# Kernel optimization log

Measured on AMD Instinct MI355X. Metric: run time of the kernel, lower is better.

Reference implementation:

```python
import jax, jax.numpy as jnp
import numpy as np

B, S, HID = 1, 2048, 2048
H, KV, D = 16, 4, 128  # head_dim = HID // H; GQA group size g = H // KV
THETA = 10000.0


def setup_inputs() -> dict:
    key = jax.random.key(0)
    ks = jax.random.split(key, 5)
    s = 0.02  # initializer_range
    return {
        "hidden_states": jax.random.normal(ks[0], (B, S, HID), jnp.float32),
        "wq": jax.random.normal(ks[1], (HID, H * D), jnp.float32) * s,
        "wk": jax.random.normal(ks[2], (HID, KV * D), jnp.float32) * s,
        "wv": jax.random.normal(ks[3], (HID, KV * D), jnp.float32) * s,
        "wo": jax.random.normal(ks[4], (H * D, HID), jnp.float32) * s,
        "attention_mask": jnp.ones((B, S), jnp.int32),
        "position_ids": jnp.broadcast_to(jnp.arange(S, dtype=jnp.int32), (B, S)),
    }


def _rope(x, position_ids):
    # x: [b, s, h, d]; rotate consecutive (even, odd) pairs by angle t * theta^{-2j/d}
    half = D // 2
    inv_freq = 1.0 / (THETA ** (jnp.arange(0, D, 2, dtype=jnp.float32) / D))  # [half]
    ang = position_ids[..., None].astype(jnp.float32) * inv_freq  # [b, s, half]
    cos = jnp.cos(ang)[:, :, None, :]  # [b, s, 1, half]
    sin = jnp.sin(ang)[:, :, None, :]
    xr = x.astype(jnp.float32).reshape(*x.shape[:-1], half, 2)
    x0, x1 = xr[..., 0], xr[..., 1]
    out = jnp.stack((x0 * cos - x1 * sin, x0 * sin + x1 * cos), axis=-1)
    return out.reshape(x.shape)


def reference(hidden_states, wq, wk, wv, wo, attention_mask, position_ids):
    b, s, _ = hidden_states.shape
    g = H // KV
    xq = (hidden_states @ wq).reshape(b, s, H, D)
    xk = (hidden_states @ wk).reshape(b, s, KV, D)
    xv = (hidden_states @ wv).reshape(b, s, KV, D)
    # GQA: each kv head repeated g consecutive times -> H heads (matches einops '(h g)')
    xk = jnp.repeat(xk, g, axis=2)
    xv = jnp.repeat(xv, g, axis=2)
    xq = _rope(xq, position_ids)
    xk = _rope(xk, position_ids)
    # causal + padding mask -> additive bias (0 or -inf), softmax in fp32
    causal = jnp.tril(jnp.ones((s, s), dtype=bool))[None, None]  # [1,1,q,k]
    mask = causal & (attention_mask[:, None, None, :] > 0)  # [b,1,q,k]
    scores = jnp.einsum('bqhd,bkhd->bhqk', xq.astype(jnp.float32), xk.astype(jnp.float32))
    scores = scores / jnp.sqrt(jnp.float32(D))
    scores = jnp.where(mask, scores, jnp.finfo(jnp.float32).min)
    attn_weights = jax.nn.softmax(scores, axis=-1)  # [b,h,q,k] fp32
    attn = jnp.einsum('bhqk,bkhd->bqhd', attn_weights, xv.astype(jnp.float32))
    return (attn.reshape(b, s, H * D).astype(hidden_states.dtype)) @ wo
```

## Files before the change

### kernel.cpp

```cpp
#include <hip/hip_runtime.h>
#include <hip/hip_bf16.h>

#define S_LEN 2048
#define HIDDIM 2048
#define NH 16
#define NKV 4
#define HD 128
#define KVROW 1024
#define QKVN 3072

typedef __attribute__((ext_vector_type(8))) short short8;
typedef __attribute__((ext_vector_type(8))) unsigned short ushort8;
typedef __attribute__((ext_vector_type(4))) unsigned short ushort4v;
typedef __attribute__((ext_vector_type(4))) float f32x4;

__device__ __forceinline__ unsigned short f2bf(float f) {
  union { float f; unsigned int u; } v; v.f = f;
  unsigned int r = (v.u + 0x7FFFu + ((v.u >> 16) & 1u)) >> 16;
  return (unsigned short)r;
}
__device__ __forceinline__ float bf2f(unsigned short h) {
  union { unsigned int u; float f; } v; v.u = ((unsigned int)h) << 16;
  return v.f;
}

__device__ __forceinline__ void gl2lds16(const unsigned short* src,
                                         unsigned short* dst) {
  __builtin_amdgcn_global_load_lds(
      (const __attribute__((address_space(1))) unsigned int*)src,
      (__attribute__((address_space(3))) unsigned int*)dst, 16, 0, 0);
}

__global__ __launch_bounds__(256) void h2b_kernel(const float* __restrict__ H,
                                                  unsigned short* __restrict__ Hb) {
  int i = (blockIdx.x * 256 + threadIdx.x) * 8;
  float4 a = *(const float4*)(H + i), b = *(const float4*)(H + i + 4);
  ushort8 r;
  r[0] = f2bf(a.x); r[1] = f2bf(a.y); r[2] = f2bf(a.z); r[3] = f2bf(a.w);
  r[4] = f2bf(b.x); r[5] = f2bf(b.y); r[6] = f2bf(b.z); r[7] = f2bf(b.w);
  *(ushort8*)(Hb + i) = r;
}

__global__ __launch_bounds__(256) void transpose_w(
    const float* __restrict__ W, unsigned short* __restrict__ Wt,
    int Nsrc, int Kdst, int n_off) {
  __shared__ unsigned short Ts[64][72];
  const int n0 = blockIdx.x * 64, k0 = blockIdx.y * 64;
  const int tid = threadIdx.x;
  const int c2 = (tid & 31) * 2, rb = tid >> 5;
#pragma unroll
  for (int p = 0; p < 8; ++p) {
    int r = rb + p * 8;
    float2 v = *(const float2*)&W[(size_t)(k0 + r) * Nsrc + n0 + c2];
    Ts[c2][r] = f2bf(v.x);
    Ts[c2 + 1][r] = f2bf(v.y);
  }
  __syncthreads();
  const int n = tid >> 2, kq = (tid & 3) * 16;
  ushort8 w0 = *(const ushort8*)&Ts[n][kq];
  ushort8 w1 = *(const ushort8*)&Ts[n][kq + 8];
  size_t base = (size_t)(n_off + n0 + n) * Kdst + k0 + kq;
  *(ushort8*)&Wt[base] = w0;
  *(ushort8*)&Wt[base + 8] = w1;
}

__global__ __launch_bounds__(256) void transpose_v(
    const unsigned short* __restrict__ KVb, unsigned short* __restrict__ Vt) {
  __shared__ unsigned short Ts[64][72];
  const int c0 = blockIdx.x * 64, s0 = blockIdx.y * 64;
  const int tid = threadIdx.x;
  const int sr = tid >> 2, cq = (tid & 3) * 16;
  ushort8 a = *(const ushort8*)&KVb[(size_t)(s0 + sr) * KVROW + 512 + c0 + cq];
  ushort8 b = *(const ushort8*)&KVb[(size_t)(s0 + sr) * KVROW + 512 + c0 + cq + 8];
#pragma unroll
  for (int j = 0; j < 8; ++j) { Ts[cq + j][sr] = a[j]; Ts[cq + 8 + j][sr] = b[j]; }
  __syncthreads();
  const int c = tid >> 2, sq = (tid & 3) * 16;
  ushort8 w0 = *(const ushort8*)&Ts[c][sq];
  ushort8 w1 = *(const ushort8*)&Ts[c][sq + 8];
  *(ushort8*)&Vt[(size_t)(c0 + c) * S_LEN + s0 + sq] = w0;
  *(ushort8*)&Vt[(size_t)(c0 + c) * S_LEN + s0 + sq + 8] = w1;
}

template <bool CF>
__global__ __launch_bounds__(256) void gemm_tn(
    const unsigned short* __restrict__ A, const unsigned short* __restrict__ Bt,
    void* __restrict__ C1, void* __restrict__ C2,
    int M, int N, int K, int splitcol, int ld1, int ld2) {
  __shared__ unsigned short As[2][128 * 64];
  __shared__ unsigned short Bs[2][64 * 64];
  const int m0 = blockIdx.y * 128, n0 = blockIdx.x * 64;
  const int tid = threadIdx.x, wid = tid >> 6, lane = tid & 63;
  const int wr = wid >> 1, wc = wid & 1;
  const int lr = lane & 15, lg = lane >> 4;

  f32x4 acc[4][2];
#pragma unroll
  for (int m = 0; m < 4; ++m)
#pragma unroll
    for (int n = 0; n < 2; ++n) acc[m][n] = (f32x4){0.f, 0.f, 0.f, 0.f};

  const int srow = lane >> 3;
  const int scolb = (lane & 7) << 4;
  auto stage = [&](int k0, int b) {
#pragma unroll
    for (int j = 0; j < 4; ++j) {
      int row = wid * 32 + j * 8 + srow;
      int src = (scolb ^ ((row & 7) << 4)) >> 1;
      gl2lds16(A + (size_t)(m0 + row) * K + k0 + src,
               &As[b][(wid * 32 + j * 8) * 64]);
    }
#pragma unroll
    for (int j = 0; j < 2; ++j) {
      int row = wid * 16 + j * 8 + srow;
      int src = (scolb ^ ((row & 7) << 4)) >> 1;
      gl2lds16(Bt + (size_t)(n0 + row) * K + k0 + src,
               &Bs[b][(wid * 16 + j * 8) * 64]);
    }
  };

  stage(0, 0);
  int cur = 0;
  for (int k0 = 0; k0 < K; k0 += 64) {
    __syncthreads();
    if (k0 + 64 < K) stage(k0 + 64, cur ^ 1);
#pragma unroll
    for (int s = 0; s < 2; ++s) {
      short8 af[4], bfv[2];
#pragma unroll
      for (int m = 0; m < 4; ++m) {
        int row = wr * 64 + m * 16 + lr;
        int off = ((s * 64 + lg * 16) ^ ((row & 7) << 4)) >> 1;
        af[m] = *(const short8*)&As[cur][row * 64 + off];
      }
#pragma unroll
      for (int n = 0; n < 2; ++n) {
        int row = wc * 32 + n * 16 + lr;
        int off = ((s * 64 + lg * 16) ^ ((row & 7) << 4)) >> 1;
        bfv[n] = *(const short8*)&Bs[cur][row * 64 + off];
      }
#pragma unroll
      for (int m = 0; m < 4; ++m)
#pragma unroll
        for (int n = 0; n < 2; ++n)
          acc[m][n] = __builtin_amdgcn_mfma_f32_16x16x32_bf16(af[m], bfv[n], acc[m][n], 0, 0, 0);
    }
    cur ^= 1;
  }

#pragma unroll
  for (int m = 0; m < 4; ++m)
#pragma unroll
    for (int n = 0; n < 2; ++n)
#pragma unroll
      for (int r = 0; r < 4; ++r) {
        int row = m0 + wr * 64 + m * 16 + lg * 4 + r;
        int col = n0 + wc * 32 + n * 16 + lr;
        float v = acc[m][n][r];
        if (CF) ((float*)C1)[(size_t)row * ld1 + col] = v;
        else if (col < splitcol) ((unsigned short*)C1)[(size_t)row * ld1 + col] = f2bf(v);
        else ((unsigned short*)C2)[(size_t)row * ld2 + (col - splitcol)] = f2bf(v);
      }
}

__global__ void rope2(unsigned short* __restrict__ Q,
                      unsigned short* __restrict__ KV,
                      const int* __restrict__ pos) {
  int idx = blockIdx.x * blockDim.x + threadIdx.x;
  if (idx >= S_LEN * 64) return;
  int s = idx >> 6, j = idx & 63;
  float inv = exp2f(-0.2076205059304703f * (float)j);
  float ang = (float)pos[s] * inv;
  float sn, cs;
  __sincosf(ang, &sn, &cs);
  auto rot = [&](unsigned short* base) {
    unsigned* p = (unsigned*)base;
    unsigned v = *p;
    float x0 = bf2f((unsigned short)(v & 0xffff));
    float x1 = bf2f((unsigned short)(v >> 16));
    unsigned r = (unsigned)f2bf(x0 * cs - x1 * sn) |
                 ((unsigned)f2bf(x0 * sn + x1 * cs) << 16);
    *p = r;
  };
#pragma unroll
  for (int hh = 0; hh < NH; ++hh) rot(Q + (size_t)s * HIDDIM + hh * HD + 2 * j);
#pragma unroll
  for (int hh = 0; hh < NKV; ++hh) rot(KV + (size_t)s * KVROW + hh * HD + 2 * j);
}

__global__ void maskbits_kernel(const int* __restrict__ amask,
                                unsigned* __restrict__ mb) {
  int w = threadIdx.x;
  unsigned m = 0;
#pragma unroll
  for (int b = 0; b < 32; ++b) m |= (amask[w * 32 + b] != 0 ? 1u : 0u) << b;
  mb[w] = m;
}

__global__ __launch_bounds__(512) void attn_kernel(
    const unsigned short* __restrict__ Qb, const unsigned short* __restrict__ KVb,
    const unsigned short* __restrict__ VtG, const unsigned* __restrict__ mbits,
    unsigned short* __restrict__ Ob,
    unsigned short* __restrict__ Opart, float* __restrict__ Lpart, int nsplit) {
  const int x = (int)blockIdx.x;
  const int qt = 63 - (x >> 2);
  const int c = x & 3;
  const int kvh = (int)blockIdx.y;
  const int nch = (qt >> 4) + 1;
  if (nsplit == 0) { if (c != 0) return; }
  else if (c >= nch) return;
  const int qb = qt * 32;
  int kbeg = 0, kend = qb + 32;
  bool partial = false;
  if (nsplit && nch > 1) {
    kbeg = c * 512;
    kend = min(kend, kbeg + 512);
    partial = true;
  }

  __shared__ unsigned short Klds[2][32 * 128];
  __shared__ unsigned short Vlds[2][128 * 32];
  __shared__ unsigned short Plds[8][16][40];
  const int tid = threadIdx.x, wid = tid >> 6, lane = tid & 63;
  const int lr = lane & 15, lg = lane >> 4;
  const int h = kvh * 4 + (wid & 3);
  const int rg = wid >> 2;
  const int qrow0 = qb + rg * 16;

  short8 qf[4];
  {
    const unsigned short* qp = Qb + (size_t)(qrow0 + lr) * HIDDIM + h * HD;
#pragma unroll
    for (int cc = 0; cc < 4; ++cc) qf[cc] = *(const short8*)(qp + cc * 32 + lg * 8);
  }
  f32x4 o[8];
#pragma unroll
  for (int cc = 0; cc < 8; ++cc) o[cc] = (f32x4){0.f, 0.f, 0.f, 0.f};
  float lsum = 0.f;

  const unsigned short* Vg = VtG + (size_t)(kvh * HD) * S_LEN;

  const int ksrow = (wid << 2) + (lane >> 4);
  const int kssrc = ((lane & 15) << 4) ^ ((ksrow & 7) << 4);
  const int vsd = (wid << 4) + (lane >> 2);
  const int vssrc = (((lane & 3) << 4) ^ ((vsd & 3) << 4));

  auto stage = [&](int kt, int b) {
    gl2lds16(KVb + (size_t)(kt + ksrow) * KVROW + kvh * HD + (kssrc >> 1),
             &Klds[b][0] + (size_t)wid * 512);
    gl2lds16(Vg + (size_t)vsd * S_LEN + kt + (vssrc >> 1),
             &Vlds[b][0] + (size_t)wid * 512);
  };

  stage(kbeg, 0);

  const int qr = qrow0 + lr;
  const float SCALE = 0.08838834764831845f;
  int cur = 0;

  for (int kt = kbeg; kt < kend; kt += 32) {
    __syncthreads();
    if (kt + 32 < kend) stage(kt + 32, cur ^ 1);

    f32x4 sc[2];
    sc[0] = (f32x4){0.f, 0.f, 0.f, 0.f};
    sc[1] = (f32x4){0.f, 0.f, 0.f, 0.f};
    const unsigned short* kbase = &Klds[cur][0];
    __builtin_amdgcn_s_setprio(1);
#pragma unroll
    for (int t = 0; t < 2; ++t)
#pragma unroll
      for (int cc = 0; cc < 4; ++cc) {
        short8 kf = *(const short8*)(kbase + ((t * 16 + lr) << 7) +
                                     ((((cc << 6) + (lg << 4)) ^ ((lr & 7) << 4)) >> 1));
        sc[t] = __builtin_amdgcn_mfma_f32_16x16x32_bf16(kf, qf[cc], sc[t], 0, 0, 0);
      }
    __builtin_amdgcn_s_setprio(0);
    const unsigned mw = mbits[kt >> 5];
    float p[2][4];
#pragma unroll
    for (int t = 0; t < 2; ++t)
#pragma unroll
      for (int r = 0; r < 4; ++r) {
        int kk = t * 16 + lg * 4 + r;
        bool ok = (kt + kk <= qr) && ((mw >> kk) & 1u);
        float s = ok ? sc[t][r] * SCALE - 3.0f : -1e30f;
        float pv = __expf(s);
        p[t][r] = pv;
        lsum += pv;
      }
#pragma unroll
    for (int t = 0; t < 2; ++t) {
      ushort4v pk;
#pragma unroll
      for (int r = 0; r < 4; ++r) pk[r] = f2bf(p[t][r]);
      *(ushort4v*)&Plds[wid][lr][t * 16 + lg * 4] = pk;
    }
    short8 pf = *(const short8*)&Plds[wid][lr][lg * 8];
    const unsigned short* vbase = &Vlds[cur][0];
    __builtin_amdgcn_s_setprio(1);
#pragma unroll
    for (int cc = 0; cc < 8; ++cc) {
      short8 vf = *(const short8*)(vbase + ((cc * 16 + lr) << 5) +
                                   ((lg ^ (lr & 3)) << 3));
      o[cc] = __builtin_amdgcn_mfma_f32_16x16x32_bf16(pf, vf, o[cc], 0, 0, 0);
    }
    __builtin_amdgcn_s_setprio(0);
    cur ^= 1;
  }

  float ls = lsum;
  ls += __shfl_xor(ls, 16, 64);
  ls += __shfl_xor(ls, 32, 64);

  if (!partial) {
    float lrec[4];
#pragma unroll
    for (int r = 0; r < 4; ++r) lrec[r] = 1.0f / __shfl(ls, lg * 4 + r, 16);
#pragma unroll
    for (int cc = 0; cc < 8; ++cc)
#pragma unroll
      for (int r = 0; r < 4; ++r) {
        const int row = qrow0 + lg * 4 + r;
        Ob[(size_t)row * HIDDIM + h * HD + cc * 16 + lr] = f2bf(o[cc][r] * lrec[r]);
      }
  } else {
    const int g = qt >> 4, j = qt & 15;
    const int base = (g == 1) ? 0 : (g == 2) ? 32 : 80;
    const int slot = base + j * nch + c + 144 * kvh;
    if (lg == 0) Lpart[slot * 128 + (wid & 3) * 32 + rg * 16 + lr] = ls;
#pragma unroll
    for (int cc = 0; cc < 8; ++cc)
#pragma unroll
      for (int r = 0; r < 4; ++r)
        Opart[(size_t)slot * 16384 + (wid & 3) * 4096 +
              (rg * 16 + lg * 4 + r) * 128 + cc * 16 + lr] = f2bf(o[cc][r]);
  }
}

__global__ __launch_bounds__(256) void combine_kernel(
    const unsigned short* __restrict__ Opart, const float* __restrict__ Lpart,
    unsigned short* __restrict__ Ab) {
  const int qt = 16 + (int)blockIdx.x;
  const int kvh = (int)blockIdx.y;
  const int nch = (qt >> 4) + 1;
  const int g = qt >> 4, j = qt & 15;
  const int base = (g == 1) ? 0 : (g == 2) ? 32 : 80;
  const int s0 = base + j * nch + 144 * kvh;
  const int tid = threadIdx.x;
  const int rowid = tid >> 1;
  const int d0 = (tid & 1) * 64;
  float L = 0.f;
  for (int cc = 0; cc < nch; ++cc) L += Lpart[(s0 + cc) * 128 + rowid];
  const float linv = 1.0f / L;
  const int h = kvh * 4 + (rowid >> 5);
  const int row = qt * 32 + (rowid & 31);
  unsigned short* dst = Ab + (size_t)row * HIDDIM + h * HD + d0;
  for (int i = 0; i < 64; i += 8) {
    float acc[8] = {0, 0, 0, 0, 0, 0, 0, 0};
    for (int cc = 0; cc < nch; ++cc) {
      ushort8 v = *(const ushort8*)&Opart[(size_t)(s0 + cc) * 16384 +
                                          rowid * 128 + d0 + i];
#pragma unroll
      for (int k = 0; k < 8; ++k) acc[k] += bf2f(v[k]);
    }
    ushort8 r;
#pragma unroll
    for (int k = 0; k < 8; ++k) r[k] = f2bf(acc[k] * linv);
    *(ushort8*)(dst + i) = r;
  }
}

extern "C" void kernel_launch(void* const* d_in, const int* in_sizes, int n_in,
                              void* d_out, int out_size, void* d_ws, size_t ws_size,
                              hipStream_t stream) {
  const float* hidden = (const float*)d_in[0];
  const float* wq = (const float*)d_in[1];
  const float* wk = (const float*)d_in[2];
  const float* wv = (const float*)d_in[3];
  const float* wo = (const float*)d_in[4];
  const int* amask = (const int*)d_in[5];
  const int* pos = (const int*)d_in[6];

  unsigned short* Qb = (unsigned short*)d_ws;
  unsigned short* KVb = Qb + (size_t)S_LEN * HIDDIM;
  unsigned short* Ab = KVb + (size_t)S_LEN * KVROW;
  unsigned short* WT1 = Ab + (size_t)S_LEN * HIDDIM;
  unsigned short* Hb = WT1 + (size_t)QKVN * HIDDIM;
  float* out = (float*)d_out;

  unsigned short* Opart = WT1;
  unsigned short* Vt_chunk = WT1 + (size_t)576 * 16384;
  unsigned* mbits_chunk = (unsigned*)((char*)d_ws + 41943040ull);
  float* Lpart = (float*)((char*)d_ws + 41943296ull);
  const size_t need_chunk = 42238208ull;
  unsigned short* Vt_fb = WT1 + (size_t)HIDDIM * HIDDIM;
  unsigned* mbits_fb = (unsigned*)((char*)d_ws + 31457280ull);

  const int nsplit = (ws_size >= need_chunk) ? 1 : 0;
  unsigned short* Vt = nsplit ? Vt_chunk : Vt_fb;
  unsigned* mbits = nsplit ? mbits_chunk : mbits_fb;

  dim3 blk(256);
  h2b_kernel<<<2048, blk, 0, stream>>>(hidden, Hb);
  transpose_w<<<dim3(32, 32), blk, 0, stream>>>(wq, WT1, HIDDIM, HIDDIM, 0);
  transpose_w<<<dim3(8, 32), blk, 0, stream>>>(wk, WT1, 512, HIDDIM, 2048);
  transpose_w<<<dim3(8, 32), blk, 0, stream>>>(wv, WT1, 512, HIDDIM, 2560);
  gemm_tn<false><<<dim3(QKVN / 64, S_LEN / 128), blk, 0, stream>>>(
      Hb, WT1, Qb, KVb, S_LEN, QKVN, HIDDIM, 2048, HIDDIM, KVROW);
  transpose_v<<<dim3(8, 32), blk, 0, stream>>>(KVb, Vt);
  rope2<<<(S_LEN * 64 + 255) / 256, blk, 0, stream>>>(Qb, KVb, pos);
  maskbits_kernel<<<1, 64, 0, stream>>>(amask, mbits);
  attn_kernel<<<dim3(256, NKV), dim3(512), 0, stream>>>(
      Qb, KVb, Vt, mbits, Ab, Opart, Lpart, nsplit);
  if (nsplit)
    combine_kernel<<<dim3(48, NKV), blk, 0, stream>>>(Opart, Lpart, Ab);
  transpose_w<<<dim3(32, 32), blk, 0, stream>>>(wo, WT1, HIDDIM, HIDDIM, 0);
  gemm_tn<true><<<dim3(HIDDIM / 64, S_LEN / 128), blk, 0, stream>>>(
      Ab, WT1, out, nullptr, S_LEN, HIDDIM, HIDDIM, HIDDIM, HIDDIM, 0);
}
```

Measured before the change: 171.4 us.

## Halve attention block to 4 waves, each handling 32 query rows per head

The attention kernel goes from 8 waves of 16 query rows to 4 waves, each covering 32 query rows of one head. Every K and V fragment read from LDS now feeds two MFMAs, which halves LDS fragment traffic per unit of work. A fast path also skips the causal and padding mask checks for key tiles fully below the diagonal with an all-ones mask. The cost is more accumulator registers per wave (two sets of 8 output tiles), which may lower occupancy, and fewer waves per block to hide latency.

```diff
diff --git a/kernel.cpp b/kernel.cpp
--- a/kernel.cpp
+++ b/kernel.cpp
@@ -197,7 +197,7 @@
   mb[w] = m;
 }
 
-__global__ __launch_bounds__(512) void attn_kernel(
+__global__ __launch_bounds__(256) void attn_kernel(
     const unsigned short* __restrict__ Qb, const unsigned short* __restrict__ KVb,
     const unsigned short* __restrict__ VtG, const unsigned* __restrict__ mbits,
     unsigned short* __restrict__ Ob,
@@ -220,41 +220,53 @@
 
   __shared__ unsigned short Klds[2][32 * 128];
   __shared__ unsigned short Vlds[2][128 * 32];
-  __shared__ unsigned short Plds[8][16][40];
+  __shared__ unsigned short Plds[4][32][40];
   const int tid = threadIdx.x, wid = tid >> 6, lane = tid & 63;
   const int lr = lane & 15, lg = lane >> 4;
-  const int h = kvh * 4 + (wid & 3);
-  const int rg = wid >> 2;
-  const int qrow0 = qb + rg * 16;
-
-  short8 qf[4];
+  const int h = kvh * 4 + wid;
+
+  short8 qfa[4], qfb[4];
   {
-    const unsigned short* qp = Qb + (size_t)(qrow0 + lr) * HIDDIM + h * HD;
-#pragma unroll
-    for (int cc = 0; cc < 4; ++cc) qf[cc] = *(const short8*)(qp + cc * 32 + lg * 8);
-  }
-  f32x4 o[8];
-#pragma unroll
-  for (int cc = 0; cc < 8; ++cc) o[cc] = (f32x4){0.f, 0.f, 0.f, 0.f};
-  float lsum = 0.f;
+    const unsigned short* qpa = Qb + (size_t)(qb + lr) * HIDDIM + h * HD;
+    const unsigned short* qpb = Qb + (size_t)(qb + 16 + lr) * HIDDIM + h * HD;
+#pragma unroll
+    for (int cc = 0; cc < 4; ++cc) {
+      qfa[cc] = *(const short8*)(qpa + cc * 32 + lg * 8);
+      qfb[cc] = *(const short8*)(qpb + cc * 32 + lg * 8);
+    }
+  }
+  f32x4 oa[8], ob[8];
+#pragma unroll
+  for (int cc = 0; cc < 8; ++cc) {
+    oa[cc] = (f32x4){0.f, 0.f, 0.f, 0.f};
+    ob[cc] = (f32x4){0.f, 0.f, 0.f, 0.f};
+  }
+  float lsa = 0.f, lsb = 0.f;
 
   const unsigned short* Vg = VtG + (size_t)(kvh * HD) * S_LEN;
 
-  const int ksrow = (wid << 2) + (lane >> 4);
-  const int kssrc = ((lane & 15) << 4) ^ ((ksrow & 7) << 4);
-  const int vsd = (wid << 4) + (lane >> 2);
-  const int vssrc = (((lane & 3) << 4) ^ ((vsd & 3) << 4));
+  const int ksr_ = lane >> 4;
+  const int kscb = (lane & 15) << 4;
+  const int vsr_ = lane >> 2;
+  const int vscb = (lane & 3) << 4;
 
   auto stage = [&](int kt, int b) {
-    gl2lds16(KVb + (size_t)(kt + ksrow) * KVROW + kvh * HD + (kssrc >> 1),
-             &Klds[b][0] + (size_t)wid * 512);
-    gl2lds16(Vg + (size_t)vsd * S_LEN + kt + (vssrc >> 1),
-             &Vlds[b][0] + (size_t)wid * 512);
+#pragma unroll
+    for (int j = 0; j < 2; ++j) {
+      int krow = wid * 8 + j * 4 + ksr_;
+      int ksrc = (kscb ^ ((krow & 7) << 4)) >> 1;
+      gl2lds16(KVb + (size_t)(kt + krow) * KVROW + kvh * HD + ksrc,
+               &Klds[b][(wid * 8 + j * 4) * 128]);
+      int vrow = wid * 32 + j * 16 + vsr_;
+      int vsrc = (vscb ^ ((vrow & 3) << 4)) >> 1;
+      gl2lds16(Vg + (size_t)vrow * S_LEN + kt + vsrc,
+               &Vlds[b][(wid * 32 + j * 16) * 32]);
+    }
   };
 
   stage(kbeg, 0);
 
-  const int qr = qrow0 + lr;
+  const int qra = qb + lr, qrb = qb + 16 + lr;
   const float SCALE = 0.08838834764831845f;
   int cur = 0;
 
@@ -262,9 +274,12 @@
     __syncthreads();
     if (kt + 32 < kend) stage(kt + 32, cur ^ 1);
 
-    f32x4 sc[2];
-    sc[0] = (f32x4){0.f, 0.f, 0.f, 0.f};
-    sc[1] = (f32x4){0.f, 0.f, 0.f, 0.f};
+    f32x4 sa[2], sb[2];
+#pragma unroll
+    for (int t = 0; t < 2; ++t) {
+      sa[t] = (f32x4){0.f, 0.f, 0.f, 0.f};
+      sb[t] = (f32x4){0.f, 0.f, 0.f, 0.f};
+    }
     const unsigned short* kbase = &Klds[cur][0];
     __builtin_amdgcn_s_setprio(1);
 #pragma unroll
@@ -273,68 +288,98 @@
       for (int cc = 0; cc < 4; ++cc) {
         short8 kf = *(const short8*)(kbase + ((t * 16 + lr) << 7) +
                                      ((((cc << 6) + (lg << 4)) ^ ((lr & 7) << 4)) >> 1));
-        sc[t] = __builtin_amdgcn_mfma_f32_16x16x32_bf16(kf, qf[cc], sc[t], 0, 0, 0);
+        sa[t] = __builtin_amdgcn_mfma_f32_16x16x32_bf16(kf, qfa[cc], sa[t], 0, 0, 0);
+        sb[t] = __builtin_amdgcn_mfma_f32_16x16x32_bf16(kf, qfb[cc], sb[t], 0, 0, 0);
       }
     __builtin_amdgcn_s_setprio(0);
     const unsigned mw = mbits[kt >> 5];
-    float p[2][4];
-#pragma unroll
-    for (int t = 0; t < 2; ++t)
-#pragma unroll
-      for (int r = 0; r < 4; ++r) {
-        int kk = t * 16 + lg * 4 + r;
-        bool ok = (kt + kk <= qr) && ((mw >> kk) & 1u);
-        float s = ok ? sc[t][r] * SCALE - 3.0f : -1e30f;
-        float pv = __expf(s);
-        p[t][r] = pv;
-        lsum += pv;
-      }
+    float pa[2][4], pb[2][4];
+    if ((kt + 31 <= qb) && (mw == ~0u)) {
+#pragma unroll
+      for (int t = 0; t < 2; ++t)
+#pragma unroll
+        for (int r = 0; r < 4; ++r) {
+          float va = __expf(sa[t][r] * SCALE - 3.0f);
+          float vb = __expf(sb[t][r] * SCALE - 3.0f);
+          pa[t][r] = va; lsa += va;
+          pb[t][r] = vb; lsb += vb;
+        }
+    } else {
+#pragma unroll
+      for (int t = 0; t < 2; ++t)
+#pragma unroll
+        for (int r = 0; r < 4; ++r) {
+          int kk = t * 16 + lg * 4 + r;
+          bool okm = (mw >> kk) & 1u;
+          float va = __expf((okm && kt + kk <= qra) ? sa[t][r] * SCALE - 3.0f : -1e30f);
+          float vb = __expf((okm && kt + kk <= qrb) ? sb[t][r] * SCALE - 3.0f : -1e30f);
+          pa[t][r] = va; lsa += va;
+          pb[t][r] = vb; lsb += vb;
+        }
+    }
 #pragma unroll
     for (int t = 0; t < 2; ++t) {
-      ushort4v pk;
-#pragma unroll
-      for (int r = 0; r < 4; ++r) pk[r] = f2bf(p[t][r]);
-      *(ushort4v*)&Plds[wid][lr][t * 16 + lg * 4] = pk;
-    }
-    short8 pf = *(const short8*)&Plds[wid][lr][lg * 8];
+      ushort4v pka, pkb;
+#pragma unroll
+      for (int r = 0; r < 4; ++r) { pka[r] = f2bf(pa[t][r]); pkb[r] = f2bf(pb[t][r]); }
+      *(ushort4v*)&Plds[wid][lr][t * 16 + lg * 4] = pka;
+      *(ushort4v*)&Plds[wid][16 + lr][t * 16 + lg * 4] = pkb;
+    }
+    short8 pfa = *(const short8*)&Plds[wid][lr][lg * 8];
+    short8 pfb = *(const short8*)&Plds[wid][16 + lr][lg * 8];
     const unsigned short* vbase = &Vlds[cur][0];
     __builtin_amdgcn_s_setprio(1);
 #pragma unroll
     for (int cc = 0; cc < 8; ++cc) {
       short8 vf = *(const short8*)(vbase + ((cc * 16 + lr) << 5) +
                                    ((lg ^ (lr & 3)) << 3));
-      o[cc] = __builtin_amdgcn_mfma_f32_16x16x32_bf16(pf, vf, o[cc], 0, 0, 0);
+      oa[cc] = __builtin_amdgcn_mfma_f32_16x16x32_bf16(pfa, vf, oa[cc], 0, 0, 0);
+      ob[cc] = __builtin_amdgcn_mfma_f32_16x16x32_bf16(pfb, vf, ob[cc], 0, 0, 0);
     }
     __builtin_amdgcn_s_setprio(0);
     cur ^= 1;
   }
 
-  float ls = lsum;
-  ls += __shfl_xor(ls, 16, 64);
-  ls += __shfl_xor(ls, 32, 64);
+  float la = lsa;
+  la += __shfl_xor(la, 16, 64);
+  la += __shfl_xor(la, 32, 64);
+  float lb = lsb;
+  lb += __shfl_xor(lb, 16, 64);
+  lb += __shfl_xor(lb, 32, 64);
 
   if (!partial) {
-    float lrec[4];
-#pragma unroll
-    for (int r = 0; r < 4; ++r) lrec[r] = 1.0f / __shfl(ls, lg * 4 + r, 16);
+    float lra[4], lrb[4];
+#pragma unroll
+    for (int r = 0; r < 4; ++r) {
+      lra[r] = 1.0f / __shfl(la, lg * 4 + r, 16);
+      lrb[r] = 1.0f / __shfl(lb, lg * 4 + r, 16);
+    }
 #pragma unroll
     for (int cc = 0; cc < 8; ++cc)
 #pragma unroll
       for (int r = 0; r < 4; ++r) {
-        const int row = qrow0 + lg * 4 + r;
-        Ob[(size_t)row * HIDDIM + h * HD + cc * 16 + lr] = f2bf(o[cc][r] * lrec[r]);
+        const int rowa = qb + lg * 4 + r;
+        const int rowb = qb + 16 + lg * 4 + r;
+        Ob[(size_t)rowa * HIDDIM + h * HD + cc * 16 + lr] = f2bf(oa[cc][r] * lra[r]);
+        Ob[(size_t)rowb * HIDDIM + h * HD + cc * 16 + lr] = f2bf(ob[cc][r] * lrb[r]);
       }
   } else {
     const int g = qt >> 4, j = qt & 15;
     const int base = (g == 1) ? 0 : (g == 2) ? 32 : 80;
     const int slot = base + j * nch + c + 144 * kvh;
-    if (lg == 0) Lpart[slot * 128 + (wid & 3) * 32 + rg * 16 + lr] = ls;
+    if (lg == 0) {
+      Lpart[slot * 128 + wid * 32 + lr] = la;
+      Lpart[slot * 128 + wid * 32 + 16 + lr] = lb;
+    }
 #pragma unroll
     for (int cc = 0; cc < 8; ++cc)
 #pragma unroll
-      for (int r = 0; r < 4; ++r)
-        Opart[(size_t)slot * 16384 + (wid & 3) * 4096 +
-              (rg * 16 + lg * 4 + r) * 128 + cc * 16 + lr] = f2bf(o[cc][r]);
+      for (int r = 0; r < 4; ++r) {
+        Opart[(size_t)slot * 16384 + wid * 4096 +
+              (lg * 4 + r) * 128 + cc * 16 + lr] = f2bf(oa[cc][r]);
+        Opart[(size_t)slot * 16384 + wid * 4096 +
+              (16 + lg * 4 + r) * 128 + cc * 16 + lr] = f2bf(ob[cc][r]);
+      }
   }
 }
 
@@ -411,7 +456,7 @@
   transpose_v<<<dim3(8, 32), blk, 0, stream>>>(KVb, Vt);
   rope2<<<(S_LEN * 64 + 255) / 256, blk, 0, stream>>>(Qb, KVb, pos);
   maskbits_kernel<<<1, 64, 0, stream>>>(amask, mbits);
-  attn_kernel<<<dim3(256, NKV), dim3(512), 0, stream>>>(
+  attn_kernel<<<dim3(256, NKV), blk, 0, stream>>>(
       Qb, KVb, Vt, mbits, Ab, Opart, Lpart, nsplit);
   if (nsplit)
     combine_kernel<<<dim3(48, NKV), blk, 0, stream>>>(Opart, Lpart, Ab);
```

Result: no change. 170.5 us (-0.5%).
